# Optimization experiments

Hardware: AMD Instinct MI355X
Metric: run time of the kernel (lower is better)

The kernel has to match this reference:

```python
import jax, jax.numpy as jnp
import numpy as np

N_HEAD = 16
D_MODEL = 1024
HEAD_DIM = D_MODEL // N_HEAD  # 64
LAMBDA_INIT = 0.8 - 0.6 * float(np.exp(-0.3 * 1))  # layer_depth = 1


def setup_inputs() -> dict:
    key = jax.random.key(0)
    ks = jax.random.split(key, 10)
    B, T, D = 1, 2048, D_MODEL
    std = 0.02
    return {
        "x": jax.random.normal(ks[0], (B, T, D), jnp.float32),
        "Wq": jax.random.normal(ks[1], (D, D), jnp.float32) * std,
        "Wk": jax.random.normal(ks[2], (D, D), jnp.float32) * std,
        "Wv": jax.random.normal(ks[3], (D, D), jnp.float32) * std,
        "Wproj": jax.random.normal(ks[4], (D, D), jnp.float32) * std,
        "lambda_q1": jax.random.normal(ks[5], (HEAD_DIM // 2,), jnp.float32) * 0.1,
        "lambda_k1": jax.random.normal(ks[6], (HEAD_DIM // 2,), jnp.float32) * 0.1,
        "lambda_q2": jax.random.normal(ks[7], (HEAD_DIM // 2,), jnp.float32) * 0.1,
        "lambda_k2": jax.random.normal(ks[8], (HEAD_DIM // 2,), jnp.float32) * 0.1,
    }


def _rms_norm(x):
    # F.rms_norm with no weight: x / sqrt(mean(x^2) + eps)
    eps = jnp.finfo(x.dtype).eps
    return x * jax.lax.rsqrt(jnp.mean(jnp.square(x), axis=-1, keepdims=True) + eps)


def _rotary_cos_sin(T, dim, base=10000.0):
    inv_freq = 1.0 / (base ** (jnp.arange(0, dim, 2, dtype=jnp.float32) / dim))
    freqs = jnp.outer(jnp.arange(T, dtype=jnp.float32), inv_freq)  # [T, dim/2]
    return jnp.cos(freqs), jnp.sin(freqs)


def _apply_rotary(x, cos, sin):
    # x: [B, T, 2, H, hd]; cos/sin: [T, hd/2] broadcast over (group, head)
    d = x.shape[-1] // 2
    c = cos[None, :, None, None, :]
    s = sin[None, :, None, None, :]
    x1, x2 = x[..., :d], x[..., d:]
    return jnp.concatenate([x1 * c + x2 * s, -x1 * s + x2 * c], axis=-1)


def _causal_attn(q, k, v, scale):
    # q,k: [B, T, H, hd]; v: [B, T, H, dv] -> [B, T, H, dv]
    T = q.shape[1]
    scores = jnp.einsum("bthd,bshd->bhts", q, k) * scale  # [B,H,T,T]
    mask = jnp.tril(jnp.ones((T, T), dtype=bool))
    scores = jnp.where(mask, scores, -jnp.inf)
    w = jax.nn.softmax(scores, axis=-1)
    return jnp.einsum("bhts,bshd->bthd", w, v)


def reference(x, Wq, Wk, Wv, Wproj, lambda_q1, lambda_k1, lambda_q2, lambda_k2):
    B, T, D = x.shape
    nh, hd = N_HEAD, HEAD_DIM
    q = (x @ Wq.T).reshape(B, T, 2, nh // 2, hd)
    k = (x @ Wk.T).reshape(B, T, 2, nh // 2, hd)
    v = (x @ Wv.T).reshape(B, T, nh // 2, 2 * hd)

    q, k = _rms_norm(q), _rms_norm(k)
    cos, sin = _rotary_cos_sin(T, hd)
    q, k = _apply_rotary(q, cos, sin), _apply_rotary(k, cos, sin)

    q1, q2 = q[:, :, 0], q[:, :, 1]
    k1, k2 = k[:, :, 0], k[:, :, 1]

    scale = 1.0 / jnp.sqrt(jnp.asarray(hd, x.dtype))
    y1 = _causal_attn(q1, k1, v, scale)  # [B,T,nh/2,2*hd]
    y2 = _causal_attn(q2, k2, v, scale)

    lambda_1 = jnp.exp(jnp.sum(lambda_q1 * lambda_k1))
    lambda_2 = jnp.exp(jnp.sum(lambda_q2 * lambda_k2))
    lambda_full = lambda_1 - lambda_2 + LAMBDA_INIT

    y = (y1 - lambda_full * y2).reshape(B, T, D)
    return y @ Wproj.T
```

## Files before the change

kernel.cpp:

```cpp
#include <hip/hip_runtime.h>
#include <hip/hip_bf16.h>

typedef __attribute__((ext_vector_type(4))) float f32x4;
typedef __attribute__((ext_vector_type(8))) short bf16x8;
typedef unsigned short u16;
typedef unsigned int u32;

#define T_SEQ 2048
#define DMODEL 1024

__device__ __forceinline__ u16 f2bf(float f) {
    __hip_bfloat16 h = __float2bfloat16(f);
    return __builtin_bit_cast(unsigned short, h);
}
__device__ __forceinline__ u16 f2h(float f) {
    _Float16 h = (_Float16)f;
    return __builtin_bit_cast(unsigned short, h);
}
__device__ __forceinline__ float h2f(u16 b) {
    return (float)__builtin_bit_cast(_Float16, b);
}

typedef const void __attribute__((address_space(1))) gvoid_t;
typedef void __attribute__((address_space(3))) lvoid_t;
__device__ __forceinline__ void gload16(const void* g, void* l) {
    __builtin_amdgcn_global_load_lds((gvoid_t*)g, (lvoid_t*)l, 16, 0, 0);
}

__device__ __forceinline__ int swz(int row, int colb) {
    return colb ^ ((row & 7) << 4);
}

__device__ __forceinline__ void cast4(const float* __restrict__ s,
                                      u16* __restrict__ d, int u) {
    int i = u * 4;
    float4 v = *(const float4*)(s + i);
    ushort4 o;
    o.x = f2bf(v.x); o.y = f2bf(v.y); o.z = f2bf(v.z); o.w = f2bf(v.w);
    *(ushort4*)(d + i) = o;
}

__global__ __launch_bounds__(256) void prep(const float* __restrict__ x,
                                            const float* __restrict__ Wq,
                                            const float* __restrict__ Wk,
                                            const float* __restrict__ Wv,
                                            const float* __restrict__ Wp,
                                            u16* __restrict__ x_bf, u16* __restrict__ wq_bf,
                                            u16* __restrict__ wk_bf, u16* __restrict__ wv_bf,
                                            u16* __restrict__ wp_bf,
                                            float* __restrict__ cosT, float* __restrict__ sinT,
                                            const float* __restrict__ lq1, const float* __restrict__ lk1,
                                            const float* __restrict__ lq2, const float* __restrict__ lk2,
                                            float* __restrict__ lam) {
    int b = blockIdx.x;
    if (b < 6144) {
        int u = b * 256 + threadIdx.x;
        if (u < 524288)       cast4(x,  x_bf,  u);
        else if (u < 786432)  cast4(Wq, wq_bf, u - 524288);
        else if (u < 1048576) cast4(Wk, wk_bf, u - 786432);
        else if (u < 1310720) cast4(Wv, wv_bf, u - 1048576);
        else                  cast4(Wp, wp_bf, u - 1310720);
    } else if (b < 6400) {
        int i = (b - 6144) * 256 + threadIdx.x;
        int t = i >> 5, j = i & 31;
        float inv = powf(10000.0f, -(float)j * (1.0f / 32.0f));
        float fr = (float)t * inv;
        cosT[i] = cosf(fr);
        sinT[i] = sinf(fr);
    } else if (threadIdx.x == 0) {
        float s1 = 0.f, s2 = 0.f;
        for (int i = 0; i < 32; ++i) { s1 += lq1[i] * lk1[i]; s2 += lq2[i] * lk2[i]; }
        *lam = expf(s1) - expf(s2) + 0.35550906759096928f;
    }
}

__device__ __forceinline__ void gemm_main64(const u16* __restrict__ A,
                                            const u16* __restrict__ B,
                                            int m0, int n0, int K,
                                            u16* lA, u16* lB, f32x4 acc[2][4]) {
    const int tid = threadIdx.x;
    const int lane = tid & 63;
    const int wid = tid >> 6;
    const int wr = (wid >> 1) * 32;
    const int wc = (wid & 1) * 64;
    const int fr = lane & 15;
    const int kc = lane >> 4;
    const char* Ab = (const char*)A;
    const char* Bb = (const char*)B;
    const int rowbytes = K * 2;

    for (int k0 = 0; k0 < K; k0 += 32) {
        {
            int c = tid;
            gload16(Ab + (size_t)(m0 + (c >> 2)) * rowbytes + k0 * 2 + (c & 3) * 16,
                    (char*)lA + c * 16);
        }
#pragma unroll
        for (int i = 0; i < 2; ++i) {
            int c = i * 256 + tid;
            gload16(Bb + (size_t)(n0 + (c >> 2)) * rowbytes + k0 * 2 + (c & 3) * 16,
                    (char*)lB + c * 16);
        }
        __syncthreads();
        bf16x8 a[2], b[4];
#pragma unroll
        for (int m = 0; m < 2; ++m) a[m] = *(const bf16x8*)&lA[(wr + m * 16 + fr) * 32 + kc * 8];
#pragma unroll
        for (int n = 0; n < 4; ++n) b[n] = *(const bf16x8*)&lB[(wc + n * 16 + fr) * 32 + kc * 8];
#pragma unroll
        for (int m = 0; m < 2; ++m)
#pragma unroll
            for (int n = 0; n < 4; ++n)
                acc[m][n] = __builtin_amdgcn_mfma_f32_16x16x32_bf16(a[m], b[n], acc[m][n], 0, 0, 0);
        __syncthreads();
    }
}

__global__ __launch_bounds__(256) void gemm_qkv(const u16* __restrict__ A,
                                                const u16* __restrict__ wq,
                                                const u16* __restrict__ wk,
                                                const u16* __restrict__ wv,
                                                const float* __restrict__ cosT,
                                                const float* __restrict__ sinT,
                                                u16* __restrict__ q_bf,
                                                u16* __restrict__ k_bf,
                                                u16* __restrict__ Vbf) {
    __shared__ __align__(16) u16 lA[64 * 32];
    __shared__ __align__(16) u16 lB[128 * 32];
    const int nt = blockIdx.x;
    const int which = nt >> 3;
    const u16* B = (which == 0) ? wq : (which == 1) ? wk : wv;
    const int m0 = blockIdx.y * 64;
    const int n0 = (nt & 7) * 128;

    f32x4 acc[2][4] = {};
    gemm_main64(A, B, m0, n0, 1024, lA, lB, acc);

    const int lane = threadIdx.x & 63;
    const int wid = threadIdx.x >> 6;
    const int wr = (wid >> 1) * 32;
    const int wc = (wid & 1) * 64;
    const int fr = lane & 15;
    const int rr = (lane >> 4) * 4;

    if (which == 2) {
#pragma unroll
        for (int m = 0; m < 2; ++m)
#pragma unroll
            for (int n = 0; n < 4; ++n)
#pragma unroll
                for (int r = 0; r < 4; ++r)
                    Vbf[(size_t)(m0 + wr + m * 16 + rr + r) * 1024 + n0 + wc + n * 16 + fr] =
                        f2bf(acc[m][n][r]);
        return;
    }

    const float oscale = (which == 0) ? 0.18033688011112042f : 1.0f;
    const int cb = n0 + wc;
    const int plane = ((cb >> 9) << 3) | ((cb >> 6) & 7);
    u16* dstp = ((which == 0) ? q_bf : k_bf) + (size_t)plane * T_SEQ * 64;
#pragma unroll
    for (int m = 0; m < 2; ++m)
#pragma unroll
        for (int r = 0; r < 4; ++r) {
            int t = m0 + wr + m * 16 + rr + r;
            float s2 = 0.f;
#pragma unroll
            for (int n = 0; n < 4; ++n) { float a = acc[m][n][r]; s2 += a * a; }
            s2 += __shfl_xor(s2, 1); s2 += __shfl_xor(s2, 2);
            s2 += __shfl_xor(s2, 4); s2 += __shfl_xor(s2, 8);
            float inv = rsqrtf(s2 * (1.0f / 64.0f) + 1.1920929e-7f);
#pragma unroll
            for (int n = 0; n < 4; ++n) {
                float a = acc[m][n][r] * inv;
                float p_ = acc[m][n ^ 2][r] * inv;
                int jj = ((n & 1) << 4) + fr;
                float c = cosT[t * 32 + jj], sn = sinT[t * 32 + jj];
                float ov = (n < 2) ? (a * c + p_ * sn) : (a * c - p_ * sn);
                dstp[(size_t)t * 64 + n * 16 + fr] = f2bf(ov * oscale);
            }
        }
}

__global__ __launch_bounds__(256) void gemm_proj(const u16* __restrict__ A,
                                                 const u16* __restrict__ B,
                                                 float* __restrict__ C) {
    __shared__ __align__(16) u16 lA[64 * 32];
    __shared__ __align__(16) u16 lB[128 * 32];
    const int m0 = blockIdx.y * 64;
    const int n0 = blockIdx.x * 128;
    f32x4 acc[2][4] = {};
    gemm_main64(A, B, m0, n0, 1024, lA, lB, acc);
    const int lane = threadIdx.x & 63;
    const int wid = threadIdx.x >> 6;
    const int wr = (wid >> 1) * 32;
    const int wc = (wid & 1) * 64;
    const int fr = lane & 15;
    const int rr = (lane >> 4) * 4;
#pragma unroll
    for (int m = 0; m < 2; ++m)
#pragma unroll
        for (int n = 0; n < 4; ++n)
#pragma unroll
            for (int r = 0; r < 4; ++r)
                C[(size_t)(m0 + wr + m * 16 + rr + r) * 1024 + (n0 + wc + n * 16 + fr)] =
                    acc[m][n][r];
}

__global__ __launch_bounds__(256) void vtrans(const u16* __restrict__ Vbf,
                                              u16* __restrict__ vT) {
    __shared__ u16 tile[32][34];
    int tx = threadIdx.x & 31;
    int ty = threadIdx.x >> 5;
    int c0 = blockIdx.x * 32;
    int r0 = blockIdx.y * 32;
#pragma unroll
    for (int i = ty; i < 32; i += 8)
        tile[i][tx] = Vbf[(size_t)(r0 + i) * 1024 + c0 + tx];
    __syncthreads();
#pragma unroll
    for (int i = ty; i < 32; i += 8)
        vT[(size_t)(c0 + i) * T_SEQ + r0 + tx] = tile[tx][i];
}

__global__ __launch_bounds__(512, 6) void attn_kernel(const u16* __restrict__ q_bf,
                                                      const u16* __restrict__ k_bf,
                                                      const u16* __restrict__ vT_bf,
                                                      u16* __restrict__ Oc,
                                                      float2* __restrict__ ml) {
    __shared__ __align__(16) u16 lK[2][64 * 64];
    __shared__ __align__(16) u16 lV[2][128 * 64];

    const int tid = threadIdx.x, lane = tid & 63, wid = tid >> 6;
    const int bid = blockIdx.x;
    const int plane = bid & 15;
    const int u = bid >> 4;
    int qt, chunk;
    if (u < 16)      { qt = 15 - (u >> 2);            chunk = u & 3; }
    else if (u < 28) { int w = u - 16; qt = 11 - w / 3; chunk = w % 3; }
    else if (u < 36) { int w = u - 28; qt = 7 - (w >> 1); chunk = w & 1; }
    else             { qt = 3 - (u - 36);             chunk = 0; }
    const int ntot = 2 * qt + 2;
    const int tb = chunk * 8;
    const int te = min(tb + 8, ntot);
    const int q0 = qt * 128;
    const int h = plane & 7;

    const u16* qp = q_bf + (size_t)plane * T_SEQ * 64;
    const char* kp = (const char*)(k_bf + (size_t)plane * T_SEQ * 64);
    const char* vp = (const char*)(vT_bf + (size_t)h * 128 * T_SEQ);
    const int fr = lane & 15, kc = lane >> 4;
    const int wsub = wid * 16;

    bf16x8 aq[2];
#pragma unroll
    for (int kq = 0; kq < 2; ++kq)
        aq[kq] = *(const bf16x8*)(qp + (size_t)(q0 + wsub + fr) * 64 + kq * 32 + kc * 8);

    f32x4 o[8] = {};
    float mi_l = -1e30f, li_l = 0.f;
    const int qrow = q0 + wsub + fr;
    const int srcA = fr + ((kc & 1) << 5);
    const int srcB = srcA + 16;
    const bool hi = kc >= 2;

    auto stage = [&](int b, int t) {
        int s0 = t << 6;
        {
            int row = tid >> 3, cp = (tid & 7) * 16;
            gload16(kp + (size_t)(s0 + row) * 128 + swz(row, cp), (char*)lK[b] + tid * 16);
        }
#pragma unroll
        for (int i = 0; i < 2; ++i) {
            int c = i * 512 + tid;
            int row = c >> 3, cp = (c & 7) * 16;
            gload16(vp + (size_t)row * (T_SEQ * 2) + (size_t)s0 * 2 + swz(row, cp),
                    (char*)lV[b] + c * 16);
        }
    };

    auto compute = [&](const char* lKb, const char* lVb, int s0, bool diag) {
        f32x4 sacc[4] = {};
        __builtin_amdgcn_s_setprio(1);
#pragma unroll
        for (int kq = 0; kq < 2; ++kq)
#pragma unroll
            for (int n = 0; n < 4; ++n) {
                int row = n * 16 + fr;
                bf16x8 bk = *(const bf16x8*)(lKb + row * 128 + swz(row, kq * 64 + kc * 16));
                sacc[n] = __builtin_amdgcn_mfma_f32_16x16x32_bf16(bk, aq[kq], sacc[n], 0, 0, 0);
            }
        __builtin_amdgcn_s_setprio(0);

        if (diag) {
#pragma unroll
            for (int n = 0; n < 4; ++n)
#pragma unroll
                for (int r = 0; r < 4; ++r)
                    if (s0 + n * 16 + kc * 4 + r > qrow) sacc[n][r] = -1e30f;
        }
        float rmax = -1e30f;
#pragma unroll
        for (int n = 0; n < 4; ++n)
#pragma unroll
            for (int r = 0; r < 4; ++r)
                rmax = fmaxf(rmax, sacc[n][r]);
        rmax = fmaxf(rmax, __shfl_xor(rmax, 16));
        rmax = fmaxf(rmax, __shfl_xor(rmax, 32));

        bool raise = rmax > mi_l + 8.0f;
        float f = raise ? __builtin_exp2f(mi_l - rmax) : 1.0f;
        if (raise) mi_l = rmax;

        float rs = 0.f;
#pragma unroll
        for (int n = 0; n < 4; ++n)
#pragma unroll
            for (int r = 0; r < 4; ++r) {
                float p = __builtin_exp2f(sacc[n][r] - mi_l);
                sacc[n][r] = p;
                rs += p;
            }
        rs += __shfl_xor(rs, 16);
        rs += __shfl_xor(rs, 32);
        li_l = li_l * f + rs;

        if (__any(raise)) {
#pragma unroll
            for (int n8 = 0; n8 < 8; ++n8)
#pragma unroll
                for (int r = 0; r < 4; ++r) o[n8][r] *= f;
        }

        u32 w32[4][2];
#pragma unroll
        for (int n = 0; n < 4; ++n)
#pragma unroll
            for (int w = 0; w < 2; ++w) {
                u32 rpk;
                asm("v_cvt_pk_bf16_f32 %0, %1, %2"
                    : "=v"(rpk) : "v"(sacc[n][2 * w]), "v"(sacc[n][2 * w + 1]));
                w32[n][w] = rpk;
            }

        __builtin_amdgcn_s_setprio(1);
#pragma unroll
        for (int kk = 0; kk < 2; ++kk) {
            u32 a0 = (u32)__shfl((int)w32[2 * kk][0], srcA);
            u32 a1 = (u32)__shfl((int)w32[2 * kk][1], srcA);
            u32 a2 = (u32)__shfl((int)w32[2 * kk][0], srcB);
            u32 a3 = (u32)__shfl((int)w32[2 * kk][1], srcB);
            u32 b0 = (u32)__shfl((int)w32[2 * kk + 1][0], srcA);
            u32 b1 = (u32)__shfl((int)w32[2 * kk + 1][1], srcA);
            u32 b2 = (u32)__shfl((int)w32[2 * kk + 1][0], srcB);
            u32 b3 = (u32)__shfl((int)w32[2 * kk + 1][1], srcB);
            union { u32 u4[4]; bf16x8 v; } ap;
            ap.u4[0] = hi ? b0 : a0;
            ap.u4[1] = hi ? b1 : a1;
            ap.u4[2] = hi ? b2 : a2;
            ap.u4[3] = hi ? b3 : a3;
#pragma unroll
            for (int n8 = 0; n8 < 8; ++n8) {
                int row = n8 * 16 + fr;
                bf16x8 bv = *(const bf16x8*)(lVb + row * 128 + swz(row, kk * 64 + kc * 16));
                o[n8] = __builtin_amdgcn_mfma_f32_16x16x32_bf16(bv, ap.v, o[n8], 0, 0, 0);
            }
        }
        __builtin_amdgcn_s_setprio(0);
    };

    stage(0, tb);
    for (int t = tb; t < te; ++t) {
        int ib = (t - tb) & 1;
        if (t + 1 < te) {
            stage(ib ^ 1, t + 1);
            asm volatile("s_waitcnt vmcnt(3)" ::: "memory");
        } else {
            asm volatile("s_waitcnt vmcnt(0)" ::: "memory");
        }
        __builtin_amdgcn_sched_barrier(0);
        __builtin_amdgcn_s_barrier();
        __builtin_amdgcn_sched_barrier(0);
        compute((const char*)lK[ib], (const char*)lV[ib], t << 6, t >= ntot - 2);
        __builtin_amdgcn_s_barrier();
    }

    const float inv_l = 1.0f / li_l;
    u16* Ob = Oc + ((size_t)(plane * 4 + chunk) * T_SEQ + qrow) * 128;
#pragma unroll
    for (int n8 = 0; n8 < 8; ++n8) {
        ushort4 w;
        w.x = f2h(o[n8][0] * inv_l);
        w.y = f2h(o[n8][1] * inv_l);
        w.z = f2h(o[n8][2] * inv_l);
        w.w = f2h(o[n8][3] * inv_l);
        *(ushort4*)(Ob + n8 * 16 + kc * 4) = w;
    }
    if (kc == 0)
        ml[(size_t)(plane * 4 + chunk) * T_SEQ + qrow] = make_float2(mi_l, li_l);
}

__global__ __launch_bounds__(256) void merge_kernel(const u16* __restrict__ Oc,
                                                    const float2* __restrict__ ml,
                                                    const float* __restrict__ lamp,
                                                    u16* __restrict__ yc) {
    int uu = blockIdx.x * 256 + threadIdx.x;
    int t = uu >> 8, rem = uu & 255, h = rem >> 5, d4 = (rem & 31) * 4;
    int qt = t >> 7;
    int nc = (qt + 4) >> 2;
    float lamv = *lamp;
    float yv[2][4];
#pragma unroll
    for (int v = 0; v < 2; ++v) {
        int plane = v * 8 + h;
        float2 m_l[4];
        float M = -1e30f;
#pragma unroll
        for (int c = 0; c < 4; ++c)
            if (c < nc) {
                m_l[c] = ml[(size_t)(plane * 4 + c) * T_SEQ + t];
                M = fmaxf(M, m_l[c].x);
            }
        float den = 0.f, a0 = 0.f, a1 = 0.f, a2 = 0.f, a3 = 0.f;
#pragma unroll
        for (int c = 0; c < 4; ++c)
            if (c < nc) {
                float w = __builtin_exp2f(m_l[c].x - M) * m_l[c].y;
                den += w;
                ushort4 ov = *(const ushort4*)(Oc +
                    ((size_t)(plane * 4 + c) * T_SEQ + t) * 128 + d4);
                a0 += w * h2f(ov.x);
                a1 += w * h2f(ov.y);
                a2 += w * h2f(ov.z);
                a3 += w * h2f(ov.w);
            }
        float inv = 1.0f / den;
        yv[v][0] = a0 * inv; yv[v][1] = a1 * inv;
        yv[v][2] = a2 * inv; yv[v][3] = a3 * inv;
    }
    ushort4 o;
    o.x = f2bf(yv[0][0] - lamv * yv[1][0]);
    o.y = f2bf(yv[0][1] - lamv * yv[1][1]);
    o.z = f2bf(yv[0][2] - lamv * yv[1][2]);
    o.w = f2bf(yv[0][3] - lamv * yv[1][3]);
    *(ushort4*)(yc + (size_t)t * 1024 + h * 128 + d4) = o;
}

extern "C" void kernel_launch(void* const* d_in, const int* in_sizes, int n_in,
                              void* d_out, int out_size, void* d_ws, size_t ws_size,
                              hipStream_t stream) {
    const float* x   = (const float*)d_in[0];
    const float* Wq  = (const float*)d_in[1];
    const float* Wk  = (const float*)d_in[2];
    const float* Wv  = (const float*)d_in[3];
    const float* Wp  = (const float*)d_in[4];
    const float* lq1 = (const float*)d_in[5];
    const float* lk1 = (const float*)d_in[6];
    const float* lq2 = (const float*)d_in[7];
    const float* lk2 = (const float*)d_in[8];
    float* out = (float*)d_out;

    char* ws = (char*)d_ws;
    u16*    x_bf  = (u16*)(ws);
    u16*    wq_bf = (u16*)(ws + (4ull << 20));
    u16*    wk_bf = (u16*)(ws + (6ull << 20));
    u16*    wv_bf = (u16*)(ws + (8ull << 20));
    u16*    wp_bf = (u16*)(ws + (10ull << 20));
    u16*    Vbf   = (u16*)(ws + (12ull << 20));
    u16*    q_bf  = (u16*)(ws + (16ull << 20));
    u16*    k_bf  = (u16*)(ws + (20ull << 20));
    u16*    vT_bf = (u16*)(ws + (24ull << 20));
    u16*    Oc    = (u16*)(ws + (28ull << 20));
    float2* ml    = (float2*)(ws + (60ull << 20));
    u16*    yc_bf = (u16*)(ws + (61ull << 20));
    float*  cosT  = (float*)(ws + (65ull << 20));
    float*  sinT  = (float*)(ws + (65ull << 20) + (256ull << 10));
    float*  lam   = (float*)(ws + (65ull << 20) + (512ull << 10));

    prep<<<6401, 256, 0, stream>>>(x, Wq, Wk, Wv, Wp,
                                   x_bf, wq_bf, wk_bf, wv_bf, wp_bf,
                                   cosT, sinT, lq1, lk1, lq2, lk2, lam);

    gemm_qkv<<<dim3(24, 32), 256, 0, stream>>>(x_bf, wq_bf, wk_bf, wv_bf,
                                               cosT, sinT, q_bf, k_bf, Vbf);

    vtrans<<<dim3(32, 64), 256, 0, stream>>>(Vbf, vT_bf);

    attn_kernel<<<640, 512, 0, stream>>>(q_bf, k_bf, vT_bf, Oc, ml);

    merge_kernel<<<2048, 256, 0, stream>>>(Oc, ml, lam, yc_bf);

    gemm_proj<<<dim3(8, 32), 256, 0, stream>>>(yc_bf, wp_bf, out);
}
```

Measured before the change: 110.8 us.

## Drop LDS staging in attention; load K/V fragments directly into registers

The attention kernel no longer stages K and V tiles through double-buffered LDS with block barriers. Each wave now loads its MFMA operand fragments straight from global memory into registers and prefetches the next K tile and the second V half in software. Blocks shrink to 256 threads with 64-row query tiles, doubling the grid, and the chunk schedule and merge kernel are updated to match. This removes LDS traffic and barriers, but each wave now issues redundant global loads, so there is more pressure on the cache and on registers.

Result: slower. 195.6 us (+76.6%).

```diff
diff --git a/kernel.cpp b/kernel.cpp
--- a/kernel.cpp
+++ b/kernel.cpp
@@ -25,10 +25,6 @@
 typedef void __attribute__((address_space(3))) lvoid_t;
 __device__ __forceinline__ void gload16(const void* g, void* l) {
     __builtin_amdgcn_global_load_lds((gvoid_t*)g, (lvoid_t*)l, 16, 0, 0);
-}
-
-__device__ __forceinline__ int swz(int row, int colb) {
-    return colb ^ ((row & 7) << 4);
 }
 
 __device__ __forceinline__ void cast4(const float* __restrict__ s,
@@ -223,76 +219,78 @@
         vT[(size_t)(c0 + i) * T_SEQ + r0 + tx] = tile[tx][i];
 }
 
-__global__ __launch_bounds__(512, 6) void attn_kernel(const u16* __restrict__ q_bf,
+__global__ __launch_bounds__(256, 3) void attn_kernel(const u16* __restrict__ q_bf,
                                                       const u16* __restrict__ k_bf,
                                                       const u16* __restrict__ vT_bf,
                                                       u16* __restrict__ Oc,
                                                       float2* __restrict__ ml) {
-    __shared__ __align__(16) u16 lK[2][64 * 64];
-    __shared__ __align__(16) u16 lV[2][128 * 64];
-
     const int tid = threadIdx.x, lane = tid & 63, wid = tid >> 6;
     const int bid = blockIdx.x;
     const int plane = bid & 15;
     const int u = bid >> 4;
     int qt, chunk;
-    if (u < 16)      { qt = 15 - (u >> 2);            chunk = u & 3; }
-    else if (u < 28) { int w = u - 16; qt = 11 - w / 3; chunk = w % 3; }
-    else if (u < 36) { int w = u - 28; qt = 7 - (w >> 1); chunk = w & 1; }
-    else             { qt = 3 - (u - 36);             chunk = 0; }
-    const int ntot = 2 * qt + 2;
+    if (u < 32)      { qt = 31 - (u >> 2);              chunk = u & 3; }
+    else if (u < 56) { int w = u - 32; qt = 23 - w / 3; chunk = w % 3; }
+    else if (u < 72) { int w = u - 56; qt = 15 - (w >> 1); chunk = w & 1; }
+    else             { qt = 7 - (u - 72);               chunk = 0; }
+    const int nt = qt + 1;
     const int tb = chunk * 8;
-    const int te = min(tb + 8, ntot);
-    const int q0 = qt * 128;
+    const int te = min(tb + 8, nt);
+    const int q0 = qt * 64;
     const int h = plane & 7;
 
+    const int fr = lane & 15, kc = lane >> 4;
+    const int qrow = q0 + wid * 16 + fr;
     const u16* qp = q_bf + (size_t)plane * T_SEQ * 64;
-    const char* kp = (const char*)(k_bf + (size_t)plane * T_SEQ * 64);
-    const char* vp = (const char*)(vT_bf + (size_t)h * 128 * T_SEQ);
-    const int fr = lane & 15, kc = lane >> 4;
-    const int wsub = wid * 16;
+    const u16* kp = k_bf + (size_t)plane * T_SEQ * 64;
+    const u16* vp = vT_bf + (size_t)h * 128 * T_SEQ;
 
     bf16x8 aq[2];
 #pragma unroll
     for (int kq = 0; kq < 2; ++kq)
-        aq[kq] = *(const bf16x8*)(qp + (size_t)(q0 + wsub + fr) * 64 + kq * 32 + kc * 8);
+        aq[kq] = *(const bf16x8*)(qp + (size_t)qrow * 64 + kq * 32 + kc * 8);
 
     f32x4 o[8] = {};
     float mi_l = -1e30f, li_l = 0.f;
-    const int qrow = q0 + wsub + fr;
     const int srcA = fr + ((kc & 1) << 5);
     const int srcB = srcA + 16;
     const bool hi = kc >= 2;
 
-    auto stage = [&](int b, int t) {
-        int s0 = t << 6;
-        {
-            int row = tid >> 3, cp = (tid & 7) * 16;
-            gload16(kp + (size_t)(s0 + row) * 128 + swz(row, cp), (char*)lK[b] + tid * 16);
-        }
-#pragma unroll
-        for (int i = 0; i < 2; ++i) {
-            int c = i * 512 + tid;
-            int row = c >> 3, cp = (c & 7) * 16;
-            gload16(vp + (size_t)row * (T_SEQ * 2) + (size_t)s0 * 2 + swz(row, cp),
-                    (char*)lV[b] + c * 16);
-        }
-    };
-
-    auto compute = [&](const char* lKb, const char* lVb, int s0, bool diag) {
+    bf16x8 bk[2][4];
+    bf16x8 bv[8];
+
+#pragma unroll
+    for (int kq = 0; kq < 2; ++kq)
+#pragma unroll
+        for (int n = 0; n < 4; ++n)
+            bk[kq][n] = *(const bf16x8*)(kp + (size_t)(tb * 64 + n * 16 + fr) * 64 +
+                                         kq * 32 + kc * 8);
+
+    for (int t = tb; t < te; ++t) {
+        const int s0 = t << 6;
+#pragma unroll
+        for (int n8 = 0; n8 < 8; ++n8)
+            bv[n8] = *(const bf16x8*)(vp + (size_t)(n8 * 16 + fr) * T_SEQ + s0 + kc * 8);
+
         f32x4 sacc[4] = {};
         __builtin_amdgcn_s_setprio(1);
 #pragma unroll
         for (int kq = 0; kq < 2; ++kq)
 #pragma unroll
-            for (int n = 0; n < 4; ++n) {
-                int row = n * 16 + fr;
-                bf16x8 bk = *(const bf16x8*)(lKb + row * 128 + swz(row, kq * 64 + kc * 16));
-                sacc[n] = __builtin_amdgcn_mfma_f32_16x16x32_bf16(bk, aq[kq], sacc[n], 0, 0, 0);
-            }
+            for (int n = 0; n < 4; ++n)
+                sacc[n] = __builtin_amdgcn_mfma_f32_16x16x32_bf16(bk[kq][n], aq[kq], sacc[n], 0, 0, 0);
         __builtin_amdgcn_s_setprio(0);
 
-        if (diag) {
+        if (t + 1 < te) {
+#pragma unroll
+            for (int kq = 0; kq < 2; ++kq)
+#pragma unroll
+                for (int n = 0; n < 4; ++n)
+                    bk[kq][n] = *(const bf16x8*)(kp + (size_t)((t + 1) * 64 + n * 16 + fr) * 64 +
+                                                 kq * 32 + kc * 8);
+        }
+
+        if (t == nt - 1) {
 #pragma unroll
             for (int n = 0; n < 4; ++n)
 #pragma unroll
@@ -343,46 +341,51 @@
                 w32[n][w] = rpk;
             }
 
-        __builtin_amdgcn_s_setprio(1);
-#pragma unroll
-        for (int kk = 0; kk < 2; ++kk) {
-            u32 a0 = (u32)__shfl((int)w32[2 * kk][0], srcA);
-            u32 a1 = (u32)__shfl((int)w32[2 * kk][1], srcA);
-            u32 a2 = (u32)__shfl((int)w32[2 * kk][0], srcB);
-            u32 a3 = (u32)__shfl((int)w32[2 * kk][1], srcB);
-            u32 b0 = (u32)__shfl((int)w32[2 * kk + 1][0], srcA);
-            u32 b1 = (u32)__shfl((int)w32[2 * kk + 1][1], srcA);
-            u32 b2 = (u32)__shfl((int)w32[2 * kk + 1][0], srcB);
-            u32 b3 = (u32)__shfl((int)w32[2 * kk + 1][1], srcB);
+        {
+            u32 a0 = (u32)__shfl((int)w32[0][0], srcA);
+            u32 a1 = (u32)__shfl((int)w32[0][1], srcA);
+            u32 a2 = (u32)__shfl((int)w32[0][0], srcB);
+            u32 a3 = (u32)__shfl((int)w32[0][1], srcB);
+            u32 b0 = (u32)__shfl((int)w32[1][0], srcA);
+            u32 b1 = (u32)__shfl((int)w32[1][1], srcA);
+            u32 b2 = (u32)__shfl((int)w32[1][0], srcB);
+            u32 b3 = (u32)__shfl((int)w32[1][1], srcB);
             union { u32 u4[4]; bf16x8 v; } ap;
             ap.u4[0] = hi ? b0 : a0;
             ap.u4[1] = hi ? b1 : a1;
             ap.u4[2] = hi ? b2 : a2;
             ap.u4[3] = hi ? b3 : a3;
-#pragma unroll
-            for (int n8 = 0; n8 < 8; ++n8) {
-                int row = n8 * 16 + fr;
-                bf16x8 bv = *(const bf16x8*)(lVb + row * 128 + swz(row, kk * 64 + kc * 16));
-                o[n8] = __builtin_amdgcn_mfma_f32_16x16x32_bf16(bv, ap.v, o[n8], 0, 0, 0);
-            }
-        }
-        __builtin_amdgcn_s_setprio(0);
-    };
-
-    stage(0, tb);
-    for (int t = tb; t < te; ++t) {
-        int ib = (t - tb) & 1;
-        if (t + 1 < te) {
-            stage(ib ^ 1, t + 1);
-            asm volatile("s_waitcnt vmcnt(3)" ::: "memory");
-        } else {
-            asm volatile("s_waitcnt vmcnt(0)" ::: "memory");
-        }
-        __builtin_amdgcn_sched_barrier(0);
-        __builtin_amdgcn_s_barrier();
-        __builtin_amdgcn_sched_barrier(0);
-        compute((const char*)lK[ib], (const char*)lV[ib], t << 6, t >= ntot - 2);
-        __builtin_amdgcn_s_barrier();
+            __builtin_amdgcn_s_setprio(1);
+#pragma unroll
+            for (int n8 = 0; n8 < 8; ++n8)
+                o[n8] = __builtin_amdgcn_mfma_f32_16x16x32_bf16(bv[n8], ap.v, o[n8], 0, 0, 0);
+            __builtin_amdgcn_s_setprio(0);
+        }
+
+#pragma unroll
+        for (int n8 = 0; n8 < 8; ++n8)
+            bv[n8] = *(const bf16x8*)(vp + (size_t)(n8 * 16 + fr) * T_SEQ + s0 + 32 + kc * 8);
+
+        {
+            u32 a0 = (u32)__shfl((int)w32[2][0], srcA);
+            u32 a1 = (u32)__shfl((int)w32[2][1], srcA);
+            u32 a2 = (u32)__shfl((int)w32[2][0], srcB);
+            u32 a3 = (u32)__shfl((int)w32[2][1], srcB);
+            u32 b0 = (u32)__shfl((int)w32[3][0], srcA);
+            u32 b1 = (u32)__shfl((int)w32[3][1], srcA);
+            u32 b2 = (u32)__shfl((int)w32[3][0], srcB);
+            u32 b3 = (u32)__shfl((int)w32[3][1], srcB);
+            union { u32 u4[4]; bf16x8 v; } ap;
+            ap.u4[0] = hi ? b0 : a0;
+            ap.u4[1] = hi ? b1 : a1;
+            ap.u4[2] = hi ? b2 : a2;
+            ap.u4[3] = hi ? b3 : a3;
+            __builtin_amdgcn_s_setprio(1);
+#pragma unroll
+            for (int n8 = 0; n8 < 8; ++n8)
+                o[n8] = __builtin_amdgcn_mfma_f32_16x16x32_bf16(bv[n8], ap.v, o[n8], 0, 0, 0);
+            __builtin_amdgcn_s_setprio(0);
+        }
     }
 
     const float inv_l = 1.0f / li_l;
@@ -406,8 +409,8 @@
                                                     u16* __restrict__ yc) {
     int uu = blockIdx.x * 256 + threadIdx.x;
     int t = uu >> 8, rem = uu & 255, h = rem >> 5, d4 = (rem & 31) * 4;
-    int qt = t >> 7;
-    int nc = (qt + 4) >> 2;
+    int qt = t >> 6;
+    int nc = (qt >> 3) + 1;
     float lamv = *lamp;
     float yv[2][4];
 #pragma unroll
@@ -486,7 +489,7 @@
 
     vtrans<<<dim3(32, 64), 256, 0, stream>>>(Vbf, vT_bf);
 
-    attn_kernel<<<640, 512, 0, stream>>>(q_bf, k_bf, vT_bf, Oc, ml);
+    attn_kernel<<<1280, 256, 0, stream>>>(q_bf, k_bf, vT_bf, Oc, ml);
 
     merge_kernel<<<2048, 256, 0, stream>>>(Oc, ml, lam, yc_bf);
 
```

## Triple-buffer LDS staging in GEMM and attention kernels with one barrier per step

Applied to the files above, without the earlier changes.

Replaces the single-buffered GEMM main loop and the double-buffered attention loop with a three-stage LDS ring. Loads for step s+2 are issued after the barrier, which removes the trailing barrier per iteration and lets global loads overlap more compute. This triples LDS use in the GEMMs and raises attention LDS from 48KB to 72KB, so the attention occupancy hint drops from 6 to 4 waves. The vmcnt(3) waits must match the per-thread load count in each stage: the GEMM stage issues 3 loads, so the count fits there, and the attention stage count is not shown.

Result: slower. 113.5 us (+2.5%).

```diff
diff --git a/kernel.cpp b/kernel.cpp
--- a/kernel.cpp
+++ b/kernel.cpp
@@ -88,31 +88,43 @@
     const char* Ab = (const char*)A;
     const char* Bb = (const char*)B;
     const int rowbytes = K * 2;
-
-    for (int k0 = 0; k0 < K; k0 += 32) {
+    const int S = K >> 5;
+
+    auto stage = [&](int s, int buf) {
         {
             int c = tid;
-            gload16(Ab + (size_t)(m0 + (c >> 2)) * rowbytes + k0 * 2 + (c & 3) * 16,
-                    (char*)lA + c * 16);
+            gload16(Ab + (size_t)(m0 + (c >> 2)) * rowbytes + s * 64 + (c & 3) * 16,
+                    (char*)(lA + buf * 2048) + c * 16);
         }
 #pragma unroll
         for (int i = 0; i < 2; ++i) {
             int c = i * 256 + tid;
-            gload16(Bb + (size_t)(n0 + (c >> 2)) * rowbytes + k0 * 2 + (c & 3) * 16,
-                    (char*)lB + c * 16);
-        }
-        __syncthreads();
+            gload16(Bb + (size_t)(n0 + (c >> 2)) * rowbytes + s * 64 + (c & 3) * 16,
+                    (char*)(lB + buf * 4096) + c * 16);
+        }
+    };
+
+    stage(0, 0);
+    if (S > 1) stage(1, 1);
+    for (int s = 0; s < S; ++s) {
+        if (s + 1 < S) asm volatile("s_waitcnt vmcnt(3)" ::: "memory");
+        else           asm volatile("s_waitcnt vmcnt(0)" ::: "memory");
+        __builtin_amdgcn_sched_barrier(0);
+        __builtin_amdgcn_s_barrier();
+        __builtin_amdgcn_sched_barrier(0);
+        if (s + 2 < S) stage(s + 2, (s + 2) % 3);
+        const u16* a_ = lA + (s % 3) * 2048;
+        const u16* b_ = lB + (s % 3) * 4096;
         bf16x8 a[2], b[4];
 #pragma unroll
-        for (int m = 0; m < 2; ++m) a[m] = *(const bf16x8*)&lA[(wr + m * 16 + fr) * 32 + kc * 8];
-#pragma unroll
-        for (int n = 0; n < 4; ++n) b[n] = *(const bf16x8*)&lB[(wc + n * 16 + fr) * 32 + kc * 8];
+        for (int m = 0; m < 2; ++m) a[m] = *(const bf16x8*)&a_[(wr + m * 16 + fr) * 32 + kc * 8];
+#pragma unroll
+        for (int n = 0; n < 4; ++n) b[n] = *(const bf16x8*)&b_[(wc + n * 16 + fr) * 32 + kc * 8];
 #pragma unroll
         for (int m = 0; m < 2; ++m)
 #pragma unroll
             for (int n = 0; n < 4; ++n)
                 acc[m][n] = __builtin_amdgcn_mfma_f32_16x16x32_bf16(a[m], b[n], acc[m][n], 0, 0, 0);
-        __syncthreads();
     }
 }
 
@@ -125,8 +137,8 @@
                                                 u16* __restrict__ q_bf,
                                                 u16* __restrict__ k_bf,
                                                 u16* __restrict__ Vbf) {
-    __shared__ __align__(16) u16 lA[64 * 32];
-    __shared__ __align__(16) u16 lB[128 * 32];
+    __shared__ __align__(16) u16 lA[3 * 64 * 32];
+    __shared__ __align__(16) u16 lB[3 * 128 * 32];
     const int nt = blockIdx.x;
     const int which = nt >> 3;
     const u16* B = (which == 0) ? wq : (which == 1) ? wk : wv;
@@ -185,8 +197,8 @@
 __global__ __launch_bounds__(256) void gemm_proj(const u16* __restrict__ A,
                                                  const u16* __restrict__ B,
                                                  float* __restrict__ C) {
-    __shared__ __align__(16) u16 lA[64 * 32];
-    __shared__ __align__(16) u16 lB[128 * 32];
+    __shared__ __align__(16) u16 lA[3 * 64 * 32];
+    __shared__ __align__(16) u16 lB[3 * 128 * 32];
     const int m0 = blockIdx.y * 64;
     const int n0 = blockIdx.x * 128;
     f32x4 acc[2][4] = {};
@@ -223,13 +235,13 @@
         vT[(size_t)(c0 + i) * T_SEQ + r0 + tx] = tile[tx][i];
 }
 
-__global__ __launch_bounds__(512, 6) void attn_kernel(const u16* __restrict__ q_bf,
+__global__ __launch_bounds__(512, 4) void attn_kernel(const u16* __restrict__ q_bf,
                                                       const u16* __restrict__ k_bf,
                                                       const u16* __restrict__ vT_bf,
                                                       u16* __restrict__ Oc,
                                                       float2* __restrict__ ml) {
-    __shared__ __align__(16) u16 lK[2][64 * 64];
-    __shared__ __align__(16) u16 lV[2][128 * 64];
+    __shared__ __align__(16) u16 lK[3][64 * 64];
+    __shared__ __align__(16) u16 lV[3][128 * 64];
 
     const int tid = threadIdx.x, lane = tid & 63, wid = tid >> 6;
     const int bid = blockIdx.x;
@@ -370,19 +382,16 @@
     };
 
     stage(0, tb);
+    if (tb + 1 < te) stage(1, tb + 1);
     for (int t = tb; t < te; ++t) {
-        int ib = (t - tb) & 1;
-        if (t + 1 < te) {
-            stage(ib ^ 1, t + 1);
-            asm volatile("s_waitcnt vmcnt(3)" ::: "memory");
-        } else {
-            asm volatile("s_waitcnt vmcnt(0)" ::: "memory");
-        }
+        if (t + 1 < te) asm volatile("s_waitcnt vmcnt(3)" ::: "memory");
+        else            asm volatile("s_waitcnt vmcnt(0)" ::: "memory");
         __builtin_amdgcn_sched_barrier(0);
         __builtin_amdgcn_s_barrier();
         __builtin_amdgcn_sched_barrier(0);
-        compute((const char*)lK[ib], (const char*)lV[ib], t << 6, t >= ntot - 2);
-        __builtin_amdgcn_s_barrier();
+        if (t + 2 < te) stage((t - tb + 2) % 3, t + 2);
+        int cb = (t - tb) % 3;
+        compute((const char*)lK[cb], (const char*)lV[cb], t << 6, t >= ntot - 2);
     }
 
     const float inv_l = 1.0f / li_l;
```

## Fuse V transpose into QKV GEMM epilogue and shrink attention tiles to 64x32

Applied to the files above, without the earlier changes.

The QKV GEMM now writes V directly in transposed layout using 4-element vector stores, which removes the separate vtrans kernel and its extra round trip through global memory. The attention kernel moves from 128-row query tiles with 64-key blocks and 8 waves to 64-row query tiles with 32-key blocks and 4 waves. The grid doubles to 1280 blocks, and the split-K chunk mapping and merge indexing are updated to match. Smaller tiles use less LDS per block and give finer load balance across the causal triangle, but each K/V tile is reused by fewer query rows and there are more barriers per key processed.

After: 102.9 us. -7.1%, faster.

```diff
diff --git a/kernel.cpp b/kernel.cpp
--- a/kernel.cpp
+++ b/kernel.cpp
@@ -25,10 +25,6 @@
 typedef void __attribute__((address_space(3))) lvoid_t;
 __device__ __forceinline__ void gload16(const void* g, void* l) {
     __builtin_amdgcn_global_load_lds((gvoid_t*)g, (lvoid_t*)l, 16, 0, 0);
-}
-
-__device__ __forceinline__ int swz(int row, int colb) {
-    return colb ^ ((row & 7) << 4);
 }
 
 __device__ __forceinline__ void cast4(const float* __restrict__ s,
@@ -124,7 +120,7 @@
                                                 const float* __restrict__ sinT,
                                                 u16* __restrict__ q_bf,
                                                 u16* __restrict__ k_bf,
-                                                u16* __restrict__ Vbf) {
+                                                u16* __restrict__ vT) {
     __shared__ __align__(16) u16 lA[64 * 32];
     __shared__ __align__(16) u16 lB[128 * 32];
     const int nt = blockIdx.x;
@@ -145,13 +141,19 @@
 
     if (which == 2) {
 #pragma unroll
-        for (int m = 0; m < 2; ++m)
-#pragma unroll
-            for (int n = 0; n < 4; ++n)
-#pragma unroll
-                for (int r = 0; r < 4; ++r)
-                    Vbf[(size_t)(m0 + wr + m * 16 + rr + r) * 1024 + n0 + wc + n * 16 + fr] =
-                        f2bf(acc[m][n][r]);
+        for (int m = 0; m < 2; ++m) {
+            int t0 = m0 + wr + m * 16 + rr;
+#pragma unroll
+            for (int n = 0; n < 4; ++n) {
+                int cb = n0 + wc + n * 16 + fr;
+                ushort4 w;
+                w.x = f2bf(acc[m][n][0]);
+                w.y = f2bf(acc[m][n][1]);
+                w.z = f2bf(acc[m][n][2]);
+                w.w = f2bf(acc[m][n][3]);
+                *(ushort4*)(vT + (size_t)cb * T_SEQ + t0) = w;
+            }
+        }
         return;
     }
 
@@ -207,101 +209,89 @@
                     acc[m][n][r];
 }
 
-__global__ __launch_bounds__(256) void vtrans(const u16* __restrict__ Vbf,
-                                              u16* __restrict__ vT) {
-    __shared__ u16 tile[32][34];
-    int tx = threadIdx.x & 31;
-    int ty = threadIdx.x >> 5;
-    int c0 = blockIdx.x * 32;
-    int r0 = blockIdx.y * 32;
-#pragma unroll
-    for (int i = ty; i < 32; i += 8)
-        tile[i][tx] = Vbf[(size_t)(r0 + i) * 1024 + c0 + tx];
-    __syncthreads();
-#pragma unroll
-    for (int i = ty; i < 32; i += 8)
-        vT[(size_t)(c0 + i) * T_SEQ + r0 + tx] = tile[tx][i];
-}
-
-__global__ __launch_bounds__(512, 6) void attn_kernel(const u16* __restrict__ q_bf,
+__global__ __launch_bounds__(256, 6) void attn_kernel(const u16* __restrict__ q_bf,
                                                       const u16* __restrict__ k_bf,
                                                       const u16* __restrict__ vT_bf,
                                                       u16* __restrict__ Oc,
                                                       float2* __restrict__ ml) {
-    __shared__ __align__(16) u16 lK[2][64 * 64];
-    __shared__ __align__(16) u16 lV[2][128 * 64];
+    __shared__ __align__(16) u16 lK[2][32 * 64];
+    __shared__ __align__(16) u16 lV[2][64 * 64];
 
     const int tid = threadIdx.x, lane = tid & 63, wid = tid >> 6;
     const int bid = blockIdx.x;
     const int plane = bid & 15;
     const int u = bid >> 4;
     int qt, chunk;
-    if (u < 16)      { qt = 15 - (u >> 2);            chunk = u & 3; }
-    else if (u < 28) { int w = u - 16; qt = 11 - w / 3; chunk = w % 3; }
-    else if (u < 36) { int w = u - 28; qt = 7 - (w >> 1); chunk = w & 1; }
-    else             { qt = 3 - (u - 36);             chunk = 0; }
+    if (u < 32)      { qt = 31 - (u >> 2);              chunk = u & 3; }
+    else if (u < 56) { int w = u - 32; qt = 23 - w / 3; chunk = w % 3; }
+    else if (u < 72) { int w = u - 56; qt = 15 - (w >> 1); chunk = w & 1; }
+    else             { qt = 7 - (u - 72);               chunk = 0; }
     const int ntot = 2 * qt + 2;
-    const int tb = chunk * 8;
-    const int te = min(tb + 8, ntot);
-    const int q0 = qt * 128;
+    const int tb = chunk * 16;
+    const int te = min(tb + 16, ntot);
+    const int q0 = qt * 64;
     const int h = plane & 7;
 
     const u16* qp = q_bf + (size_t)plane * T_SEQ * 64;
     const char* kp = (const char*)(k_bf + (size_t)plane * T_SEQ * 64);
     const char* vp = (const char*)(vT_bf + (size_t)h * 128 * T_SEQ);
     const int fr = lane & 15, kc = lane >> 4;
-    const int wsub = wid * 16;
+    const int qrow = q0 + wid * 16 + fr;
 
     bf16x8 aq[2];
 #pragma unroll
     for (int kq = 0; kq < 2; ++kq)
-        aq[kq] = *(const bf16x8*)(qp + (size_t)(q0 + wsub + fr) * 64 + kq * 32 + kc * 8);
+        aq[kq] = *(const bf16x8*)(qp + (size_t)qrow * 64 + kq * 32 + kc * 8);
 
     f32x4 o[8] = {};
     float mi_l = -1e30f, li_l = 0.f;
-    const int qrow = q0 + wsub + fr;
     const int srcA = fr + ((kc & 1) << 5);
     const int srcB = srcA + 16;
     const bool hi = kc >= 2;
 
     auto stage = [&](int b, int t) {
-        int s0 = t << 6;
+        int s0 = t << 5;
         {
             int row = tid >> 3, cp = (tid & 7) * 16;
-            gload16(kp + (size_t)(s0 + row) * 128 + swz(row, cp), (char*)lK[b] + tid * 16);
+            gload16(kp + (size_t)(s0 + row) * 128 + (cp ^ ((row & 7) << 4)),
+                    (char*)lK[b] + tid * 16);
         }
 #pragma unroll
         for (int i = 0; i < 2; ++i) {
-            int c = i * 512 + tid;
-            int row = c >> 3, cp = (c & 7) * 16;
-            gload16(vp + (size_t)row * (T_SEQ * 2) + (size_t)s0 * 2 + swz(row, cp),
+            int c = i * 256 + tid;
+            int row = c >> 3, cb = (c & 7) * 16;
+            int cbs = cb ^ ((row & 7) << 4);
+            int d = row * 2 + (cbs >> 6);
+            int kk = (cbs & 63) >> 1;
+            gload16(vp + (size_t)d * (T_SEQ * 2) + (size_t)(s0 + kk) * 2,
                     (char*)lV[b] + c * 16);
         }
     };
 
     auto compute = [&](const char* lKb, const char* lVb, int s0, bool diag) {
-        f32x4 sacc[4] = {};
+        f32x4 sacc[2] = {};
         __builtin_amdgcn_s_setprio(1);
 #pragma unroll
         for (int kq = 0; kq < 2; ++kq)
 #pragma unroll
-            for (int n = 0; n < 4; ++n) {
+            for (int n = 0; n < 2; ++n) {
                 int row = n * 16 + fr;
-                bf16x8 bk = *(const bf16x8*)(lKb + row * 128 + swz(row, kq * 64 + kc * 16));
+                bf16x8 bk = *(const bf16x8*)(lKb + row * 128 +
+                                             ((kq * 64 + kc * 16) ^ ((row & 7) << 4)));
                 sacc[n] = __builtin_amdgcn_mfma_f32_16x16x32_bf16(bk, aq[kq], sacc[n], 0, 0, 0);
             }
         __builtin_amdgcn_s_setprio(0);
 
         if (diag) {
 #pragma unroll
-            for (int n = 0; n < 4; ++n)
+            for (int n = 0; n < 2; ++n)
 #pragma unroll
                 for (int r = 0; r < 4; ++r)
                     if (s0 + n * 16 + kc * 4 + r > qrow) sacc[n][r] = -1e30f;
         }
         float rmax = -1e30f;
 #pragma unroll
-        for (int n = 0; n < 4; ++n)
+        for (int n = 0; n < 2; ++n)
 #pragma unroll
             for (int r = 0; r < 4; ++r)
                 rmax = fmaxf(rmax, sacc[n][r]);
@@ -314,7 +304,7 @@
 
         float rs = 0.f;
 #pragma unroll
-        for (int n = 0; n < 4; ++n)
+        for (int n = 0; n < 2; ++n)
 #pragma unroll
             for (int r = 0; r < 4; ++r) {
                 float p = __builtin_exp2f(sacc[n][r] - mi_l);
@@ -332,9 +322,9 @@
                 for (int r = 0; r < 4; ++r) o[n8][r] *= f;
         }
 
-        u32 w32[4][2];
-#pragma unroll
-        for (int n = 0; n < 4; ++n)
+        u32 w32[2][2];
+#pragma unroll
+        for (int n = 0; n < 2; ++n)
 #pragma unroll
             for (int w = 0; w < 2; ++w) {
                 u32 rpk;
@@ -343,28 +333,28 @@
                 w32[n][w] = rpk;
             }
 
+        u32 a0 = (u32)__shfl((int)w32[0][0], srcA);
+        u32 a1 = (u32)__shfl((int)w32[0][1], srcA);
+        u32 a2 = (u32)__shfl((int)w32[0][0], srcB);
+        u32 a3 = (u32)__shfl((int)w32[0][1], srcB);
+        u32 b0 = (u32)__shfl((int)w32[1][0], srcA);
+        u32 b1 = (u32)__shfl((int)w32[1][1], srcA);
+        u32 b2 = (u32)__shfl((int)w32[1][0], srcB);
+        u32 b3 = (u32)__shfl((int)w32[1][1], srcB);
+        union { u32 u4[4]; bf16x8 v; } ap;
+        ap.u4[0] = hi ? b0 : a0;
+        ap.u4[1] = hi ? b1 : a1;
+        ap.u4[2] = hi ? b2 : a2;
+        ap.u4[3] = hi ? b3 : a3;
+
         __builtin_amdgcn_s_setprio(1);
 #pragma unroll
-        for (int kk = 0; kk < 2; ++kk) {
-            u32 a0 = (u32)__shfl((int)w32[2 * kk][0], srcA);
-            u32 a1 = (u32)__shfl((int)w32[2 * kk][1], srcA);
-            u32 a2 = (u32)__shfl((int)w32[2 * kk][0], srcB);
-            u32 a3 = (u32)__shfl((int)w32[2 * kk][1], srcB);
-            u32 b0 = (u32)__shfl((int)w32[2 * kk + 1][0], srcA);
-            u32 b1 = (u32)__shfl((int)w32[2 * kk + 1][1], srcA);
-            u32 b2 = (u32)__shfl((int)w32[2 * kk + 1][0], srcB);
-            u32 b3 = (u32)__shfl((int)w32[2 * kk + 1][1], srcB);
-            union { u32 u4[4]; bf16x8 v; } ap;
-            ap.u4[0] = hi ? b0 : a0;
-            ap.u4[1] = hi ? b1 : a1;
-            ap.u4[2] = hi ? b2 : a2;
-            ap.u4[3] = hi ? b3 : a3;
-#pragma unroll
-            for (int n8 = 0; n8 < 8; ++n8) {
-                int row = n8 * 16 + fr;
-                bf16x8 bv = *(const bf16x8*)(lVb + row * 128 + swz(row, kk * 64 + kc * 16));
-                o[n8] = __builtin_amdgcn_mfma_f32_16x16x32_bf16(bv, ap.v, o[n8], 0, 0, 0);
-            }
+        for (int n8 = 0; n8 < 8; ++n8) {
+            int d = n8 * 16 + fr;
+            int row = d >> 1;
+            int colb = (d & 1) * 64 + kc * 16;
+            bf16x8 bv = *(const bf16x8*)(lVb + row * 128 + (colb ^ ((row & 7) << 4)));
+            o[n8] = __builtin_amdgcn_mfma_f32_16x16x32_bf16(bv, ap.v, o[n8], 0, 0, 0);
         }
         __builtin_amdgcn_s_setprio(0);
     };
@@ -381,7 +371,7 @@
         __builtin_amdgcn_sched_barrier(0);
         __builtin_amdgcn_s_barrier();
         __builtin_amdgcn_sched_barrier(0);
-        compute((const char*)lK[ib], (const char*)lV[ib], t << 6, t >= ntot - 2);
+        compute((const char*)lK[ib], (const char*)lV[ib], t << 5, t >= ntot - 2);
         __builtin_amdgcn_s_barrier();
     }
 
@@ -406,8 +396,8 @@
                                                     u16* __restrict__ yc) {
     int uu = blockIdx.x * 256 + threadIdx.x;
     int t = uu >> 8, rem = uu & 255, h = rem >> 5, d4 = (rem & 31) * 4;
-    int qt = t >> 7;
-    int nc = (qt + 4) >> 2;
+    int qt = t >> 6;
+    int nc = (qt + 8) >> 3;
     float lamv = *lamp;
     float yv[2][4];
 #pragma unroll
@@ -466,27 +456,24 @@
     u16*    wk_bf = (u16*)(ws + (6ull << 20));
     u16*    wv_bf = (u16*)(ws + (8ull << 20));
     u16*    wp_bf = (u16*)(ws + (10ull << 20));
-    u16*    Vbf   = (u16*)(ws + (12ull << 20));
+    u16*    vT_bf = (u16*)(ws + (12ull << 20));
     u16*    q_bf  = (u16*)(ws + (16ull << 20));
     u16*    k_bf  = (u16*)(ws + (20ull << 20));
-    u16*    vT_bf = (u16*)(ws + (24ull << 20));
-    u16*    Oc    = (u16*)(ws + (28ull << 20));
-    float2* ml    = (float2*)(ws + (60ull << 20));
-    u16*    yc_bf = (u16*)(ws + (61ull << 20));
-    float*  cosT  = (float*)(ws + (65ull << 20));
-    float*  sinT  = (float*)(ws + (65ull << 20) + (256ull << 10));
-    float*  lam   = (float*)(ws + (65ull << 20) + (512ull << 10));
+    u16*    Oc    = (u16*)(ws + (24ull << 20));
+    float2* ml    = (float2*)(ws + (56ull << 20));
+    u16*    yc_bf = (u16*)(ws + (57ull << 20));
+    float*  cosT  = (float*)(ws + (61ull << 20));
+    float*  sinT  = (float*)(ws + (61ull << 20) + (256ull << 10));
+    float*  lam   = (float*)(ws + (61ull << 20) + (512ull << 10));
 
     prep<<<6401, 256, 0, stream>>>(x, Wq, Wk, Wv, Wp,
                                    x_bf, wq_bf, wk_bf, wv_bf, wp_bf,
                                    cosT, sinT, lq1, lk1, lq2, lk2, lam);
 
     gemm_qkv<<<dim3(24, 32), 256, 0, stream>>>(x_bf, wq_bf, wk_bf, wv_bf,
-                                               cosT, sinT, q_bf, k_bf, Vbf);
-
-    vtrans<<<dim3(32, 64), 256, 0, stream>>>(Vbf, vT_bf);
-
-    attn_kernel<<<640, 512, 0, stream>>>(q_bf, k_bf, vT_bf, Oc, ml);
+                                               cosT, sinT, q_bf, k_bf, vT_bf);
+
+    attn_kernel<<<1280, 256, 0, stream>>>(q_bf, k_bf, vT_bf, Oc, ml);
 
     merge_kernel<<<2048, 256, 0, stream>>>(Oc, ml, lam, yc_bf);
 
```
